# Performance work log

Hardware: AMD Instinct MI355X
Metric: run time of the kernel (lower is better)

The kernel has to match this reference:

```python
import jax, jax.numpy as jnp
import numpy as np

B, S, R, L, Z = 2048, 277, 80, 12, 56


def setup_inputs() -> dict:
    key = jax.random.key(0)
    k0, k1, k2, k3, k4, k5 = jax.random.split(key, 6)
    true_idx = jax.random.randint(k0, (B, S), 0, R)
    x = jax.nn.one_hot(true_idx, R, dtype=jnp.float32)            # one-hot true rules
    recon_x = jax.nn.softmax(jax.random.normal(k1, (B, S, R)), axis=-1)  # post-softmax probs
    mu = jax.random.normal(k2, (B, Z), dtype=jnp.float32)
    log_var = jax.random.normal(k3, (B, Z), dtype=jnp.float32)
    ind_to_lhs_ind = jax.random.randint(k4, (R,), 0, L)
    masks = (jax.random.uniform(k5, (L, R)) > 0.5).astype(jnp.float32)
    # a valid grammar always allows the true rule under its own LHS mask
    masks = masks.at[ind_to_lhs_ind, jnp.arange(R)].set(1.0)
    return {"x": x, "recon_x": recon_x, "mu": mu, "log_var": log_var,
            "masks": masks, "ind_to_lhs_ind": ind_to_lhs_ind}


def reference(x, recon_x, mu, log_var, masks, ind_to_lhs_ind):
    batch_size, seq_len, n_rules = x.shape
    z_size = mu.shape[1]
    # apply_masks: fused gather + mask + renormalize (replaces B*S python loop)
    true_rule = jnp.argmax(x, axis=-1)                 # [B,S]
    mask = masks[ind_to_lhs_ind[true_rule]]            # [B,S,R]
    x_resc = recon_x * mask
    out = x_resc / jnp.sum(x_resc, axis=-1, keepdims=True)
    # BCELoss(size_average=False): torch clamps log terms at -100
    log_p = jnp.clip(jnp.log(out), -100.0, None)
    log_1mp = jnp.clip(jnp.log1p(-out), -100.0, None)
    bce = -jnp.sum(x * log_p + (1.0 - x) * log_1mp) / (seq_len * batch_size)
    # sample_z == False branch: moment-matching error
    avg_mu = jnp.sum(mu, axis=0) / batch_size          # [Z]
    var = jnp.matmul(mu.T, mu) / batch_size            # [Z,Z]
    var_err = var - jnp.eye(z_size, dtype=mu.dtype)
    mom_err = jnp.sum(avg_mu * avg_mu) / z_size + jnp.sum(jnp.abs(var_err)) / (z_size * z_size)
    return bce + mom_err
```

## Files before the change

kernel.cpp:

```cpp
#include <hip/hip_runtime.h>
#include <math.h>

#define Bn 2048
#define Sn 277
#define Rn 80
#define Ln 12
#define Zn 56
#define NROWS (Bn * Sn)
#define NBLK1 (NROWS / 256)


#define BITAT(jj) ((((jj) < 32 ? (b0 >> (jj)) : ((jj) < 64 ? (b1 >> ((jj) - 32)) : (b2 >> ((jj) - 64)))) & 1u) != 0u)

__global__ __launch_bounds__(256) void bce_kernel(
    const float* __restrict__ x, const float* __restrict__ recon,
    const float* __restrict__ masks, const int* __restrict__ lhs_ind,
    double* __restrict__ bce_partial)
{
    __shared__ unsigned int sbits[Ln][4];
    __shared__ int slhs[Rn];
    __shared__ float swsum[4];

    const int tid = threadIdx.x;

    if (tid < Ln * 3) {
        int l = tid / 3, w = tid % 3;
        unsigned int bits = 0u;
        for (int b = 0; b < 32; ++b) {
            int j = w * 32 + b;
            if (j < Rn && masks[l * Rn + j] > 0.5f) bits |= (1u << b);
        }
        sbits[l][w] = bits;
    }
    if (tid < Rn) slhs[tid] = lhs_ind[tid];
    __syncthreads();

    const int row = blockIdx.x * 256 + tid;

    const float4* xp = (const float4*)(x + (size_t)row * Rn);
    int amax = 0;
    #pragma unroll
    for (int k = 0; k < 20; ++k) {
        float4 v = xp[k];
        if (v.x > 0.5f) amax = 4 * k + 0;
        if (v.y > 0.5f) amax = 4 * k + 1;
        if (v.z > 0.5f) amax = 4 * k + 2;
        if (v.w > 0.5f) amax = 4 * k + 3;
    }
    const int l = slhs[amax];
    const unsigned int b0 = sbits[l][0], b1 = sbits[l][1], b2 = sbits[l][2];

    float vals[Rn];
    float denom = 0.0f;
    const float4* rp = (const float4*)(recon + (size_t)row * Rn);
    #pragma unroll
    for (int k = 0; k < 20; ++k) {
        float4 v = rp[k];
        const int j = 4 * k;
        float e0 = BITAT(j + 0) ? v.x : 0.0f;
        float e1 = BITAT(j + 1) ? v.y : 0.0f;
        float e2 = BITAT(j + 2) ? v.z : 0.0f;
        float e3 = BITAT(j + 3) ? v.w : 0.0f;
        vals[j + 0] = e0; vals[j + 1] = e1; vals[j + 2] = e2; vals[j + 3] = e3;
        denom += (e0 + e1) + (e2 + e3);
    }

    const float invd = 1.0f / denom;
    float ta = 1.0f;
    float ssum = 0.0f;
    #pragma unroll
    for (int j = 0; j < Rn; ++j) {
        float t = vals[j] * invd;
        t = fminf(t, 1.0f);
        ssum += fmaxf(__logf(1.0f - t), -100.0f);
        ta = (j == amax) ? t : ta;
    }
    const float la  = fmaxf(__logf(ta), -100.0f);
    const float lpa = fmaxf(__logf(1.0f - ta), -100.0f);
    float contrib = (ssum - lpa) + la;

    #pragma unroll
    for (int o = 32; o > 0; o >>= 1) contrib += __shfl_down(contrib, o, 64);
    if ((tid & 63) == 0) swsum[tid >> 6] = contrib;
    __syncthreads();
    if (tid == 0)
        bce_partial[blockIdx.x] = (double)((swsum[0] + swsum[1]) + (swsum[2] + swsum[3]));
}

__global__ __launch_bounds__(256) void moments_kernel(
    const float* __restrict__ mu, float* __restrict__ ws_var, float* __restrict__ ws_avg)
{
    __shared__ float sm[64 * Zn];
    const int tid = threadIdx.x;
    const int r0 = blockIdx.x * 64;

    for (int i = tid; i < 64 * Zn; i += 256) sm[i] = mu[(size_t)r0 * Zn + i];
    __syncthreads();

    for (int p = tid; p < Zn * Zn; p += 256) {
        int i = p / Zn, j = p % Zn;
        float acc = 0.0f;
        for (int r = 0; r < 64; ++r) acc = fmaf(sm[r * Zn + i], sm[r * Zn + j], acc);
        atomicAdd(&ws_var[p], acc);
    }
    if (tid < Zn) {
        float acc = 0.0f;
        for (int r = 0; r < 64; ++r) acc += sm[r * Zn + tid];
        atomicAdd(&ws_avg[tid], acc);
    }
}

__global__ __launch_bounds__(256) void finalize_kernel(
    const double* __restrict__ bce_partial, const float* __restrict__ ws_var,
    const float* __restrict__ ws_avg, float* __restrict__ out)
{
    __shared__ double sb[4];
    __shared__ float sv[4], sa[4];
    const int tid = threadIdx.x;

    double bsum = 0.0;
    for (int i = tid; i < NBLK1; i += 256) bsum += bce_partial[i];

    float vsum = 0.0f;
    for (int p = tid; p < Zn * Zn; p += 256) {
        int i = p / Zn, j = p % Zn;
        float v = ws_var[p] * (1.0f / (float)Bn) - ((i == j) ? 1.0f : 0.0f);
        vsum += fabsf(v);
    }
    float asum = 0.0f;
    for (int z = tid; z < Zn; z += 256) { float a = ws_avg[z]; asum += a * a; }

    #pragma unroll
    for (int o = 32; o > 0; o >>= 1) {
        bsum += __shfl_down(bsum, o, 64);
        vsum += __shfl_down(vsum, o, 64);
        asum += __shfl_down(asum, o, 64);
    }
    if ((tid & 63) == 0) { int w = tid >> 6; sb[w] = bsum; sv[w] = vsum; sa[w] = asum; }
    __syncthreads();
    if (tid == 0) {
        double tb = (sb[0] + sb[1]) + (sb[2] + sb[3]);
        double tv = (double)((sv[0] + sv[1]) + (sv[2] + sv[3]));
        double ta = (double)((sa[0] + sa[1]) + (sa[2] + sa[3]));
        double bce = -tb / ((double)Sn * (double)Bn);
        double mom = ta / ((double)Bn * (double)Bn * (double)Zn)
                   + tv / ((double)Zn * (double)Zn);
        out[0] = (float)(bce + mom);
    }
}

extern "C" void kernel_launch(void* const* d_in, const int* in_sizes, int n_in,
                              void* d_out, int out_size, void* d_ws, size_t ws_size,
                              hipStream_t stream)
{
    const float* x     = (const float*)d_in[0];
    const float* recon = (const float*)d_in[1];
    const float* mu    = (const float*)d_in[2];
    const float* masks = (const float*)d_in[4];
    const int*   lhs   = (const int*)d_in[5];
    float* out = (float*)d_out;

    char* ws = (char*)d_ws;
    double* bce_partial = (double*)ws;
    float* ws_avg = (float*)(ws + 17728);
    float* ws_var = (float*)(ws + 17952);

    hipMemsetAsync(ws + 17728, 0, 224 + 12544, stream);

    bce_kernel<<<NBLK1, 256, 0, stream>>>(x, recon, masks, lhs, bce_partial);
    moments_kernel<<<Bn / 64, 256, 0, stream>>>(mu, ws_var, ws_avg);
    finalize_kernel<<<1, 256, 0, stream>>>(bce_partial, ws_var, ws_avg, out);
}
```

Before: 406.8 us.

## Coalesce BCE row loads across 16-lane groups and fuse moments into one launch

The BCE kernel now gives each row to a group of 16 lanes, which load contiguous float4 chunks and combine the argmax and denominator with shuffles. This replaces the one-thread-per-row strided loads and the 80-float register array. Mask bit packing moves to a tiny setup kernel. The moments computation runs as extra blocks of the same launch and writes per-block partials instead of atomics, which removes the memset. The cost is more shuffles per row and a heavier finalize, plus the risk that the 8 moment blocks become a tail.

```diff
diff --git a/kernel.cpp b/kernel.cpp
--- a/kernel.cpp
+++ b/kernel.cpp
@@ -7,144 +7,223 @@
 #define Ln 12
 #define Zn 56
 #define NROWS (Bn * Sn)
-#define NBLK1 (NROWS / 256)
-
-
-#define BITAT(jj) ((((jj) < 32 ? (b0 >> (jj)) : ((jj) < 64 ? (b1 >> ((jj) - 32)) : (b2 >> ((jj) - 64)))) & 1u) != 0u)
-
-__global__ __launch_bounds__(256) void bce_kernel(
+#define ROWS_PER_BLK 64
+#define NBLK_BCE (NROWS / ROWS_PER_BLK)
+#define NMOM 8
+#define NBLK_TOT (NBLK_BCE + NMOM)
+
+#define WS_SBITS 0
+#define WS_LHS   192
+#define WS_BCE   512
+#define WS_VAR   71424
+#define WS_AVG   171776
+
+__global__ __launch_bounds__(128) void setup_kernel(
+    const float* __restrict__ masks, const int* __restrict__ lhs, char* __restrict__ ws)
+{
+    unsigned* sbits_g = (unsigned*)(ws + WS_SBITS);
+    int* lhs_g = (int*)(ws + WS_LHS);
+    const int t = threadIdx.x;
+    if (t < Ln * 4) {
+        const int l = t >> 2, w = t & 3;
+        unsigned bits = 0u;
+        if (w < 3) {
+            for (int b = 0; b < 32; ++b) {
+                const int j = w * 32 + b;
+                if (j < Rn && masks[l * Rn + j] > 0.5f) bits |= (1u << b);
+            }
+        }
+        sbits_g[t] = bits;
+    }
+    if (t >= 48 && t < 48 + Rn) lhs_g[t - 48] = lhs[t - 48];
+}
+
+__global__ __launch_bounds__(256) void main_kernel(
     const float* __restrict__ x, const float* __restrict__ recon,
-    const float* __restrict__ masks, const int* __restrict__ lhs_ind,
-    double* __restrict__ bce_partial)
-{
-    __shared__ unsigned int sbits[Ln][4];
-    __shared__ int slhs[Rn];
-    __shared__ float swsum[4];
-
+    const float* __restrict__ mu, char* __restrict__ ws)
+{
     const int tid = threadIdx.x;
 
-    if (tid < Ln * 3) {
-        int l = tid / 3, w = tid % 3;
-        unsigned int bits = 0u;
-        for (int b = 0; b < 32; ++b) {
-            int j = w * 32 + b;
-            if (j < Rn && masks[l * Rn + j] > 0.5f) bits |= (1u << b);
-        }
-        sbits[l][w] = bits;
-    }
-    if (tid < Rn) slhs[tid] = lhs_ind[tid];
-    __syncthreads();
-
-    const int row = blockIdx.x * 256 + tid;
-
-    const float4* xp = (const float4*)(x + (size_t)row * Rn);
-    int amax = 0;
-    #pragma unroll
-    for (int k = 0; k < 20; ++k) {
-        float4 v = xp[k];
-        if (v.x > 0.5f) amax = 4 * k + 0;
-        if (v.y > 0.5f) amax = 4 * k + 1;
-        if (v.z > 0.5f) amax = 4 * k + 2;
-        if (v.w > 0.5f) amax = 4 * k + 3;
-    }
-    const int l = slhs[amax];
-    const unsigned int b0 = sbits[l][0], b1 = sbits[l][1], b2 = sbits[l][2];
-
-    float vals[Rn];
-    float denom = 0.0f;
-    const float4* rp = (const float4*)(recon + (size_t)row * Rn);
-    #pragma unroll
-    for (int k = 0; k < 20; ++k) {
-        float4 v = rp[k];
-        const int j = 4 * k;
-        float e0 = BITAT(j + 0) ? v.x : 0.0f;
-        float e1 = BITAT(j + 1) ? v.y : 0.0f;
-        float e2 = BITAT(j + 2) ? v.z : 0.0f;
-        float e3 = BITAT(j + 3) ? v.w : 0.0f;
-        vals[j + 0] = e0; vals[j + 1] = e1; vals[j + 2] = e2; vals[j + 3] = e3;
-        denom += (e0 + e1) + (e2 + e3);
-    }
-
-    const float invd = 1.0f / denom;
-    float ta = 1.0f;
-    float ssum = 0.0f;
-    #pragma unroll
-    for (int j = 0; j < Rn; ++j) {
-        float t = vals[j] * invd;
-        t = fminf(t, 1.0f);
-        ssum += fmaxf(__logf(1.0f - t), -100.0f);
-        ta = (j == amax) ? t : ta;
-    }
-    const float la  = fmaxf(__logf(ta), -100.0f);
-    const float lpa = fmaxf(__logf(1.0f - ta), -100.0f);
-    float contrib = (ssum - lpa) + la;
-
-    #pragma unroll
-    for (int o = 32; o > 0; o >>= 1) contrib += __shfl_down(contrib, o, 64);
-    if ((tid & 63) == 0) swsum[tid >> 6] = contrib;
-    __syncthreads();
-    if (tid == 0)
-        bce_partial[blockIdx.x] = (double)((swsum[0] + swsum[1]) + (swsum[2] + swsum[3]));
-}
-
-__global__ __launch_bounds__(256) void moments_kernel(
-    const float* __restrict__ mu, float* __restrict__ ws_var, float* __restrict__ ws_avg)
-{
-    __shared__ float sm[64 * Zn];
-    const int tid = threadIdx.x;
-    const int r0 = blockIdx.x * 64;
-
-    for (int i = tid; i < 64 * Zn; i += 256) sm[i] = mu[(size_t)r0 * Zn + i];
-    __syncthreads();
-
-    for (int p = tid; p < Zn * Zn; p += 256) {
-        int i = p / Zn, j = p % Zn;
-        float acc = 0.0f;
-        for (int r = 0; r < 64; ++r) acc = fmaf(sm[r * Zn + i], sm[r * Zn + j], acc);
-        atomicAdd(&ws_var[p], acc);
-    }
-    if (tid < Zn) {
-        float acc = 0.0f;
-        for (int r = 0; r < 64; ++r) acc += sm[r * Zn + tid];
-        atomicAdd(&ws_avg[tid], acc);
+    if (blockIdx.x < NBLK_BCE) {
+        const unsigned* sbits_g = (const unsigned*)(ws + WS_SBITS);
+        const int* lhs_g = (const int*)(ws + WS_LHS);
+        double* bce_partial = (double*)(ws + WS_BCE);
+
+        __shared__ unsigned sbits[Ln * 4];
+        __shared__ int slhs[Rn];
+        __shared__ float swsum[4];
+
+        if (tid < Ln * 4) sbits[tid] = sbits_g[tid];
+        else if (tid >= 64 && tid < 64 + Rn) slhs[tid - 64] = lhs_g[tid - 64];
+        __syncthreads();
+
+        const int grp = tid >> 4;
+        const int sl  = tid & 15;
+        float contrib = 0.0f;
+
+        for (int it = 0; it < 4; ++it) {
+            const int row = blockIdx.x * ROWS_PER_BLK + it * 16 + grp;
+            const float4* xp = (const float4*)(x + (size_t)row * Rn);
+            const float4* rp = (const float4*)(recon + (size_t)row * Rn);
+
+            float4 xv = xp[sl];
+            float4 rv = rp[sl];
+            float4 xe = make_float4(0.f, 0.f, 0.f, 0.f);
+            float4 re = make_float4(0.f, 0.f, 0.f, 0.f);
+            if (sl < 4) { xe = xp[16 + sl]; re = rp[16 + sl]; }
+
+            const int jb = 4 * sl;
+            const int je = 64 + 4 * sl;
+            int cand = -1;
+            if (xv.x > 0.5f) cand = jb;
+            if (xv.y > 0.5f) cand = jb + 1;
+            if (xv.z > 0.5f) cand = jb + 2;
+            if (xv.w > 0.5f) cand = jb + 3;
+            if (xe.x > 0.5f) cand = je;
+            if (xe.y > 0.5f) cand = je + 1;
+            if (xe.z > 0.5f) cand = je + 2;
+            if (xe.w > 0.5f) cand = je + 3;
+            cand = max(cand, __shfl_xor(cand, 1));
+            cand = max(cand, __shfl_xor(cand, 2));
+            cand = max(cand, __shfl_xor(cand, 4));
+            cand = max(cand, __shfl_xor(cand, 8));
+            const int amax = cand;
+
+            const int l = slhs[amax];
+            const unsigned bw = sbits[l * 4 + (sl >> 3)];
+            const unsigned b2 = sbits[l * 4 + 2];
+            const int sh = 4 * (sl & 7);
+
+            const float v0 = ((bw >> (sh + 0)) & 1u) ? rv.x : 0.f;
+            const float v1 = ((bw >> (sh + 1)) & 1u) ? rv.y : 0.f;
+            const float v2 = ((bw >> (sh + 2)) & 1u) ? rv.z : 0.f;
+            const float v3 = ((bw >> (sh + 3)) & 1u) ? rv.w : 0.f;
+            const float e0 = ((b2 >> (sh + 0)) & 1u) ? re.x : 0.f;
+            const float e1 = ((b2 >> (sh + 1)) & 1u) ? re.y : 0.f;
+            const float e2 = ((b2 >> (sh + 2)) & 1u) ? re.z : 0.f;
+            const float e3 = ((b2 >> (sh + 3)) & 1u) ? re.w : 0.f;
+
+            float d = ((v0 + v1) + (v2 + v3)) + ((e0 + e1) + (e2 + e3));
+            d += __shfl_xor(d, 1);
+            d += __shfl_xor(d, 2);
+            d += __shfl_xor(d, 4);
+            d += __shfl_xor(d, 8);
+            const float invd = 1.0f / d;
+
+            float ta = -1.0f;
+            float ss = 0.0f;
+            {
+                float t;
+                t = fminf(v0 * invd, 1.f); ss += fmaxf(__logf(1.f - t), -100.f); if (jb + 0 == amax) ta = t;
+                t = fminf(v1 * invd, 1.f); ss += fmaxf(__logf(1.f - t), -100.f); if (jb + 1 == amax) ta = t;
+                t = fminf(v2 * invd, 1.f); ss += fmaxf(__logf(1.f - t), -100.f); if (jb + 2 == amax) ta = t;
+                t = fminf(v3 * invd, 1.f); ss += fmaxf(__logf(1.f - t), -100.f); if (jb + 3 == amax) ta = t;
+                t = fminf(e0 * invd, 1.f); ss += fmaxf(__logf(1.f - t), -100.f); if (je + 0 == amax) ta = t;
+                t = fminf(e1 * invd, 1.f); ss += fmaxf(__logf(1.f - t), -100.f); if (je + 1 == amax) ta = t;
+                t = fminf(e2 * invd, 1.f); ss += fmaxf(__logf(1.f - t), -100.f); if (je + 2 == amax) ta = t;
+                t = fminf(e3 * invd, 1.f); ss += fmaxf(__logf(1.f - t), -100.f); if (je + 3 == amax) ta = t;
+            }
+            if (ta >= 0.0f)
+                ss += fmaxf(__logf(ta), -100.f) - fmaxf(__logf(1.f - ta), -100.f);
+            contrib += ss;
+        }
+
+        #pragma unroll
+        for (int m = 32; m; m >>= 1) contrib += __shfl_xor(contrib, m);
+        if ((tid & 63) == 0) swsum[tid >> 6] = contrib;
+        __syncthreads();
+        if (tid == 0)
+            bce_partial[blockIdx.x] = (double)((swsum[0] + swsum[1]) + (swsum[2] + swsum[3]));
+    } else {
+        float* var_partial = (float*)(ws + WS_VAR);
+        float* avg_partial = (float*)(ws + WS_AVG);
+        __shared__ float sm[64 * Zn];
+
+        const int m = blockIdx.x - NBLK_BCE;
+        float acc[13];
+        #pragma unroll
+        for (int k = 0; k < 13; ++k) acc[k] = 0.0f;
+        float asum = 0.0f;
+
+        for (int c = 0; c < 4; ++c) {
+            __syncthreads();
+            const float* src = mu + ((size_t)m * 256 + c * 64) * Zn;
+            for (int i = tid; i < 64 * Zn; i += 256) sm[i] = src[i];
+            __syncthreads();
+
+            #pragma unroll
+            for (int k = 0; k < 13; ++k) {
+                const int p = tid + 256 * k;
+                if (p < Zn * Zn) {
+                    const int i = p / Zn, j = p - i * Zn;
+                    float a = 0.0f;
+                    #pragma unroll 8
+                    for (int r = 0; r < 64; ++r) a = fmaf(sm[r * Zn + i], sm[r * Zn + j], a);
+                    acc[k] += a;
+                }
+            }
+            if (tid < Zn) {
+                float s = 0.0f;
+                #pragma unroll 8
+                for (int r = 0; r < 64; ++r) s += sm[r * Zn + tid];
+                asum += s;
+            }
+        }
+        #pragma unroll
+        for (int k = 0; k < 13; ++k) {
+            const int p = tid + 256 * k;
+            if (p < Zn * Zn) var_partial[m * (Zn * Zn) + p] = acc[k];
+        }
+        if (tid < Zn) avg_partial[m * Zn + tid] = asum;
     }
 }
 
 __global__ __launch_bounds__(256) void finalize_kernel(
-    const double* __restrict__ bce_partial, const float* __restrict__ ws_var,
-    const float* __restrict__ ws_avg, float* __restrict__ out)
-{
+    const char* __restrict__ ws, float* __restrict__ out)
+{
+    const double* bce_partial = (const double*)(ws + WS_BCE);
+    const float* var_partial = (const float*)(ws + WS_VAR);
+    const float* avg_partial = (const float*)(ws + WS_AVG);
     __shared__ double sb[4];
     __shared__ float sv[4], sa[4];
     const int tid = threadIdx.x;
 
     double bsum = 0.0;
-    for (int i = tid; i < NBLK1; i += 256) bsum += bce_partial[i];
+    for (int i = tid; i < NBLK_BCE; i += 256) bsum += bce_partial[i];
 
     float vsum = 0.0f;
     for (int p = tid; p < Zn * Zn; p += 256) {
-        int i = p / Zn, j = p % Zn;
-        float v = ws_var[p] * (1.0f / (float)Bn) - ((i == j) ? 1.0f : 0.0f);
-        vsum += fabsf(v);
-    }
+        float v = 0.0f;
+        #pragma unroll
+        for (int m = 0; m < NMOM; ++m) v += var_partial[m * (Zn * Zn) + p];
+        const int i = p / Zn, j = p - i * Zn;
+        const float e = v * (1.0f / (float)Bn) - ((i == j) ? 1.0f : 0.0f);
+        vsum += fabsf(e);
+    }
+
     float asum = 0.0f;
-    for (int z = tid; z < Zn; z += 256) { float a = ws_avg[z]; asum += a * a; }
+    for (int z = tid; z < Zn; z += 256) {
+        float a = 0.0f;
+        #pragma unroll
+        for (int m = 0; m < NMOM; ++m) a += avg_partial[m * Zn + z];
+        asum += a * a;
+    }
 
     #pragma unroll
-    for (int o = 32; o > 0; o >>= 1) {
+    for (int o = 32; o; o >>= 1) {
         bsum += __shfl_down(bsum, o, 64);
         vsum += __shfl_down(vsum, o, 64);
         asum += __shfl_down(asum, o, 64);
     }
-    if ((tid & 63) == 0) { int w = tid >> 6; sb[w] = bsum; sv[w] = vsum; sa[w] = asum; }
+    if ((tid & 63) == 0) { const int w = tid >> 6; sb[w] = bsum; sv[w] = vsum; sa[w] = asum; }
     __syncthreads();
     if (tid == 0) {
-        double tb = (sb[0] + sb[1]) + (sb[2] + sb[3]);
-        double tv = (double)((sv[0] + sv[1]) + (sv[2] + sv[3]));
-        double ta = (double)((sa[0] + sa[1]) + (sa[2] + sa[3]));
-        double bce = -tb / ((double)Sn * (double)Bn);
-        double mom = ta / ((double)Bn * (double)Bn * (double)Zn)
-                   + tv / ((double)Zn * (double)Zn);
+        const double tb = (sb[0] + sb[1]) + (sb[2] + sb[3]);
+        const double tv = (double)((sv[0] + sv[1]) + (sv[2] + sv[3]));
+        const double ta = (double)((sa[0] + sa[1]) + (sa[2] + sa[3]));
+        const double bce = -tb / ((double)Sn * (double)Bn);
+        const double mom = ta / ((double)Bn * (double)Bn * (double)Zn)
+                         + tv / ((double)Zn * (double)Zn);
         out[0] = (float)(bce + mom);
     }
 }
@@ -159,15 +238,9 @@
     const float* masks = (const float*)d_in[4];
     const int*   lhs   = (const int*)d_in[5];
     float* out = (float*)d_out;
-
     char* ws = (char*)d_ws;
-    double* bce_partial = (double*)ws;
-    float* ws_avg = (float*)(ws + 17728);
-    float* ws_var = (float*)(ws + 17952);
-
-    hipMemsetAsync(ws + 17728, 0, 224 + 12544, stream);
-
-    bce_kernel<<<NBLK1, 256, 0, stream>>>(x, recon, masks, lhs, bce_partial);
-    moments_kernel<<<Bn / 64, 256, 0, stream>>>(mu, ws_var, ws_avg);
-    finalize_kernel<<<1, 256, 0, stream>>>(bce_partial, ws_var, ws_avg, out);
-}
+
+    setup_kernel<<<1, 128, 0, stream>>>(masks, lhs, ws);
+    main_kernel<<<NBLK_TOT, 256, 0, stream>>>(x, recon, mu, ws);
+    finalize_kernel<<<1, 256, 0, stream>>>(ws, out);
+}
```

New measurement: 459.5 us. +13.0%, slower.
